# Performance work log

Measured on AMD Instinct MI355X. Metric: run time of the kernel, lower is better.

## Reference

```python
import jax, jax.numpy as jnp
import numpy as np

B, D, K = 32768, 256, 1024


def setup_inputs() -> dict:
    key = jax.random.key(0)
    k1, k2 = jax.random.split(key)
    embedding = jax.random.normal(k1, (B, D), dtype=jnp.float32)
    codebook = jax.random.normal(k2, (K, D), dtype=jnp.float32)
    return {"embedding": embedding, "codebook": codebook}


def reference(embedding, codebook):
    # code_norms: (K,) squared L2 norm of each code
    code_norms = jnp.sum(codebook ** 2, axis=1)            # (K,)
    dots = embedding @ codebook.T                           # (B, K)
    alpha = dots / code_norms[None, :]                      # (B, K)
    # error for projecting e onto line of code c:
    #   ||e - alpha c||^2 = ||e||^2 - dots^2 / ||c||^2
    # (identical math to materializing (B,K,D) diff, without the blowup)
    e_norms = jnp.sum(embedding ** 2, axis=1, keepdims=True)  # (B, 1)
    errors = e_norms - dots ** 2 / code_norms[None, :]        # (B, K)
    indices = jnp.argmin(errors, axis=1)                      # (B,)
    # gather chosen projection: alpha[b, idx[b]] * codebook[idx[b]]
    alpha_sel = jnp.take_along_axis(alpha, indices[:, None], axis=1)  # (B, 1)
    z_out = alpha_sel * codebook[indices]                     # (B, D)
    return (z_out, indices)
```

## Files before the change

kernel.cpp:

```cpp
#include <hip/hip_runtime.h>
#include <cstdint>

#define B_ROWS 32768
#define DIM    256
#define KCODES 1024
#define NSPLIT 2

typedef _Float16 f16x8 __attribute__((ext_vector_type(8)));
typedef float    f32x4 __attribute__((ext_vector_type(4)));


__global__ __launch_bounds__(64) void vq_prep(const float* __restrict__ cb,
                                              _Float16* __restrict__ hi,
                                              _Float16* __restrict__ lo,
                                              float* __restrict__ inv_norm) {
  const int k = blockIdx.x;
  const int lane = threadIdx.x;
  float4 c = reinterpret_cast<const float4*>(cb)[k * 64 + lane];
  float nrm = c.x * c.x + c.y * c.y + c.z * c.z + c.w * c.w;
#pragma unroll
  for (int off = 32; off; off >>= 1) nrm += __shfl_xor(nrm, off);
  if (lane == 0) inv_norm[k] = 1.0f / nrm;

  float f[4] = {c.x, c.y, c.z, c.w};
  _Float16 h[4], l[4];
#pragma unroll
  for (int i = 0; i < 4; ++i) {
    h[i] = (_Float16)f[i];
    l[i] = (_Float16)((f[i] - (float)h[i]) * 2048.0f);
  }
  const int phys = (lane >> 1) ^ (k & 15);
  const int byteoff = k * 512 + phys * 16 + (lane & 1) * 8;
  *reinterpret_cast<uint2*>((char*)hi + byteoff) = *reinterpret_cast<uint2*>(h);
  *reinterpret_cast<uint2*>((char*)lo + byteoff) = *reinterpret_cast<uint2*>(l);
}

__device__ __forceinline__ void gld16(const void* g, void* l) {
  __builtin_amdgcn_global_load_lds(
      (const __attribute__((address_space(1))) uint32_t*)g,
      (__attribute__((address_space(3))) uint32_t*)l, 16, 0, 0);
}

__global__ __launch_bounds__(256, 1) void vq_main(const float* __restrict__ emb,
                                                  const _Float16* __restrict__ cbh,
                                                  const _Float16* __restrict__ cbl,
                                                  const float* __restrict__ inv_g,
                                                  float2* __restrict__ cand) {
  __shared__ uint4 Btile[2][1024];
  __shared__ float inv_s[KCODES];

  const int flat = threadIdx.x;
  const int wave = flat >> 6;
  const int lane = flat & 63;
  const int quad = lane >> 4;
  const int lr   = lane & 15;

  const int split  = blockIdx.x & (NSPLIT - 1);
  const int rowblk = blockIdx.x >> 1;
  const int t0 = split * 32;

  reinterpret_cast<float4*>(inv_s)[flat] = reinterpret_cast<const float4*>(inv_g)[flat];

  f16x8 Ah[4][8], Al[4][8];
  const int row0 = rowblk * 256 + wave * 64;
#pragma unroll
  for (int s = 0; s < 4; ++s) {
    const float* rp = emb + (size_t)(row0 + s * 16 + lr) * DIM;
#pragma unroll
    for (int c = 0; c < 8; ++c) {
      const float* p = rp + c * 32 + quad * 8;
      float4 f0 = *reinterpret_cast<const float4*>(p);
      float4 f1 = *reinterpret_cast<const float4*>(p + 4);
      float f[8] = {f0.x, f0.y, f0.z, f0.w, f1.x, f1.y, f1.z, f1.w};
      f16x8 h, l;
#pragma unroll
      for (int j = 0; j < 8; ++j) {
        _Float16 hv = (_Float16)f[j];
        h[j] = hv;
        l[j] = (_Float16)((f[j] - (float)hv) * 2048.0f);
      }
      Ah[s][c] = h;
      Al[s][c] = l;
    }
  }

  auto stage = [&](int buf, int t) {
    const char* srcH = (const char*)cbh + t * 8192;
    const char* srcL = (const char*)cbl + t * 8192;
    char* dst = (char*)&Btile[buf][0];
    const int off = flat * 16;
    gld16(srcH + off,        dst + off);
    gld16(srcH + 4096 + off, dst + 4096 + off);
    gld16(srcL + off,        dst + 8192 + off);
    gld16(srcL + 4096 + off, dst + 12288 + off);
  };
  stage(0, t0);

  float bg[16], bd[16];
  int   bk[16];
#pragma unroll
  for (int i = 0; i < 16; ++i) { bg[i] = -1.0f; bd[i] = 0.0f; bk[i] = t0 * 16; }

  auto comp = [&](const char* buf, f32x4* aA, f32x4* aB) {
#pragma unroll
    for (int s = 0; s < 4; ++s) {
      aA[s] = (f32x4){0, 0, 0, 0};
      aB[s] = (f32x4){0, 0, 0, 0};
    }
#pragma unroll
    for (int c = 0; c < 8; ++c) {
      const int g = (((c * 4 + quad) ^ lr) * 16) + lr * 512;
      f16x8 bh = *reinterpret_cast<const f16x8*>(buf + g);
      f16x8 bl = *reinterpret_cast<const f16x8*>(buf + 8192 + g);
#pragma unroll
      for (int s = 0; s < 4; ++s) {
        aA[s] = __builtin_amdgcn_mfma_f32_16x16x32_f16(Ah[s][c], bh, aA[s], 0, 0, 0);
        aB[s] = __builtin_amdgcn_mfma_f32_16x16x32_f16(Al[s][c], bh, aB[s], 0, 0, 0);
        aB[s] = __builtin_amdgcn_mfma_f32_16x16x32_f16(Ah[s][c], bl, aB[s], 0, 0, 0);
      }
    }
  };

  auto epi = [&](const f32x4* aA, const f32x4* aB, int t) {
    const int n = t * 16 + lr;
    const float inl = inv_s[n];
#pragma unroll
    for (int s = 0; s < 4; ++s)
#pragma unroll
      for (int r = 0; r < 4; ++r) {
        float d = fmaf(aB[s][r], 4.8828125e-4f, aA[s][r]);
        float g = d * d * inl;
        const int i = (s << 2) | r;
        if (g > bg[i]) { bg[i] = g; bd[i] = d; bk[i] = n; }
      }
  };

  f32x4 aA0[4], aB0[4], aA1[4], aB1[4];
  for (int tt = 0; tt < 32; tt += 2) {
    __syncthreads();
    stage(1, t0 + tt + 1);
    comp((const char*)&Btile[0][0], aA0, aB0);
    if (tt) epi(aA1, aB1, t0 + tt - 1);
    __syncthreads();
    if (tt + 2 < 32) stage(0, t0 + tt + 2);
    comp((const char*)&Btile[1][0], aA1, aB1);
    epi(aA0, aB0, t0 + tt);
  }
  epi(aA1, aB1, t0 + 31);

#pragma unroll
  for (int s = 0; s < 4; ++s) {
#pragma unroll
    for (int r = 0; r < 4; ++r) {
      const int i = (s << 2) | r;
      float g = bg[i]; int k = bk[i]; float d = bd[i];
#pragma unroll
      for (int m = 1; m < 16; m <<= 1) {
        float g2 = __shfl_xor(g, m);
        int   k2 = __shfl_xor(k, m);
        float d2 = __shfl_xor(d, m);
        if (g2 > g || (g2 == g && k2 < k)) { g = g2; k = k2; d = d2; }
      }
      if (lr == 0) {
        const int row = row0 + s * 16 + quad * 4 + r;
        cand[(size_t)split * B_ROWS + row] = make_float2(d, __int_as_float(k));
      }
    }
  }
}

__global__ __launch_bounds__(256) void vq_reduce(const float2* __restrict__ cand,
                                                 const float* __restrict__ inv_g,
                                                 const float* __restrict__ cb,
                                                 float* __restrict__ out) {
  const int wave = threadIdx.x >> 6;
  const int lane = threadIdx.x & 63;
  const int row = blockIdx.x * 4 + wave;

  float best_g = -1.0f, best_d = 0.0f;
  int best_k = 0;
#pragma unroll
  for (int s = 0; s < NSPLIT; ++s) {
    float2 c = cand[(size_t)s * B_ROWS + row];
    int k = __float_as_int(c.y);
    float g = c.x * c.x * inv_g[k];
    if (g > best_g || (g == best_g && k < best_k)) {
      best_g = g; best_d = c.x; best_k = k;
    }
  }
  const float alpha = best_d * inv_g[best_k];
  float4 c4 = reinterpret_cast<const float4*>(cb)[best_k * 64 + lane];
  float4 z = {alpha * c4.x, alpha * c4.y, alpha * c4.z, alpha * c4.w};
  reinterpret_cast<float4*>(out)[(size_t)row * 64 + lane] = z;
  if (lane == 0) out[(size_t)B_ROWS * DIM + row] = (float)best_k;
}

extern "C" void kernel_launch(void* const* d_in, const int* in_sizes, int n_in,
                              void* d_out, int out_size, void* d_ws, size_t ws_size,
                              hipStream_t stream) {
  const float* emb = (const float*)d_in[0];
  const float* cb  = (const float*)d_in[1];
  _Float16* cbh = (_Float16*)d_ws;
  _Float16* cbl = (_Float16*)((char*)d_ws + (512 << 10));
  float*    inv = (float*)((char*)d_ws + (1 << 20));
  float2*   cand = (float2*)((char*)d_ws + (1 << 20) + 4096);

  vq_prep<<<KCODES, 64, 0, stream>>>(cb, cbh, cbl, inv);
  vq_main<<<(B_ROWS / 256) * NSPLIT, 256, 0, stream>>>(emb, cbh, cbl, inv, cand);
  vq_reduce<<<B_ROWS / 4, 256, 0, stream>>>(cand, inv, cb, (float*)d_out);
}
```

Before: 158.3 us.

## Pre-normalize codebook, drop per-code scaling, double tile size and split accumulators

The codebook is pre-scaled by 1/||c|| in the prep kernel, so the main kernel compares squared dots directly. This removes the inverse-norm shared table and its per-tile multiply, and the reduce kernel rescales alpha using the stored inverse sqrt norm. The main loop now stages 32 codes per barrier instead of 16, halving the number of syncs. It also uses three independent accumulator chains instead of two to shorten MFMA dependency chains. The trade-offs are a larger LDS footprint, extra accumulator registers, and slightly different rounding from normalizing before the fp16 hi/lo split.

```diff
diff --git a/kernel.cpp b/kernel.cpp
--- a/kernel.cpp
+++ b/kernel.cpp
@@ -13,16 +13,17 @@
 __global__ __launch_bounds__(64) void vq_prep(const float* __restrict__ cb,
                                               _Float16* __restrict__ hi,
                                               _Float16* __restrict__ lo,
-                                              float* __restrict__ inv_norm) {
+                                              float* __restrict__ ivs) {
   const int k = blockIdx.x;
   const int lane = threadIdx.x;
   float4 c = reinterpret_cast<const float4*>(cb)[k * 64 + lane];
   float nrm = c.x * c.x + c.y * c.y + c.z * c.z + c.w * c.w;
 #pragma unroll
   for (int off = 32; off; off >>= 1) nrm += __shfl_xor(nrm, off);
-  if (lane == 0) inv_norm[k] = 1.0f / nrm;
-
-  float f[4] = {c.x, c.y, c.z, c.w};
+  const float invn = 1.0f / sqrtf(nrm);
+  if (lane == 0) ivs[k] = invn;
+
+  float f[4] = {c.x * invn, c.y * invn, c.z * invn, c.w * invn};
   _Float16 h[4], l[4];
 #pragma unroll
   for (int i = 0; i < 4; ++i) {
@@ -44,10 +45,8 @@
 __global__ __launch_bounds__(256, 1) void vq_main(const float* __restrict__ emb,
                                                   const _Float16* __restrict__ cbh,
                                                   const _Float16* __restrict__ cbl,
-                                                  const float* __restrict__ inv_g,
                                                   float2* __restrict__ cand) {
-  __shared__ uint4 Btile[2][1024];
-  __shared__ float inv_s[KCODES];
+  __shared__ uint4 Btile[2][2048];
 
   const int flat = threadIdx.x;
   const int wave = flat >> 6;
@@ -57,9 +56,7 @@
 
   const int split  = blockIdx.x & (NSPLIT - 1);
   const int rowblk = blockIdx.x >> 1;
-  const int t0 = split * 32;
-
-  reinterpret_cast<float4*>(inv_s)[flat] = reinterpret_cast<const float4*>(inv_g)[flat];
+  const int code0  = split * 512;
 
   f16x8 Ah[4][8], Al[4][8];
   const int row0 = rowblk * 256 + wave * 64;
@@ -84,69 +81,68 @@
     }
   }
 
-  auto stage = [&](int buf, int t) {
-    const char* srcH = (const char*)cbh + t * 8192;
-    const char* srcL = (const char*)cbl + t * 8192;
+  auto stage = [&](int buf, int ch) {
+    const int cbase = code0 + ch * 32;
     char* dst = (char*)&Btile[buf][0];
-    const int off = flat * 16;
-    gld16(srcH + off,        dst + off);
-    gld16(srcH + 4096 + off, dst + 4096 + off);
-    gld16(srcL + off,        dst + 8192 + off);
-    gld16(srcL + 4096 + off, dst + 12288 + off);
+    const int off = wave * 2048 + lane * 16;
+#pragma unroll
+    for (int r = 0; r < 4; ++r) {
+      const char* src = (const char*)((r & 1) ? cbl : cbh) + (cbase + (r >> 1) * 16) * 512;
+      gld16(src + off,        dst + r * 8192 + off);
+      gld16(src + off + 1024, dst + r * 8192 + off + 1024);
+    }
   };
-  stage(0, t0);
+  stage(0, 0);
 
   float bg[16], bd[16];
   int   bk[16];
 #pragma unroll
-  for (int i = 0; i < 16; ++i) { bg[i] = -1.0f; bd[i] = 0.0f; bk[i] = t0 * 16; }
-
-  auto comp = [&](const char* buf, f32x4* aA, f32x4* aB) {
-#pragma unroll
-    for (int s = 0; s < 4; ++s) {
-      aA[s] = (f32x4){0, 0, 0, 0};
-      aB[s] = (f32x4){0, 0, 0, 0};
-    }
-#pragma unroll
-    for (int c = 0; c < 8; ++c) {
-      const int g = (((c * 4 + quad) ^ lr) * 16) + lr * 512;
-      f16x8 bh = *reinterpret_cast<const f16x8*>(buf + g);
-      f16x8 bl = *reinterpret_cast<const f16x8*>(buf + 8192 + g);
+  for (int i = 0; i < 16; ++i) { bg[i] = -1.0f; bd[i] = 0.0f; bk[i] = code0; }
+
+  __syncthreads();
+  for (int ch = 0; ch < 16; ++ch) {
+    const char* base = (const char*)&Btile[ch & 1][0];
+    if (ch + 1 < 16) stage((ch + 1) & 1, ch + 1);
+
+#pragma unroll
+    for (int tt = 0; tt < 2; ++tt) {
+      f32x4 aA[4], aB[4], aC[4];
 #pragma unroll
       for (int s = 0; s < 4; ++s) {
-        aA[s] = __builtin_amdgcn_mfma_f32_16x16x32_f16(Ah[s][c], bh, aA[s], 0, 0, 0);
-        aB[s] = __builtin_amdgcn_mfma_f32_16x16x32_f16(Al[s][c], bh, aB[s], 0, 0, 0);
-        aB[s] = __builtin_amdgcn_mfma_f32_16x16x32_f16(Ah[s][c], bl, aB[s], 0, 0, 0);
-      }
-    }
-  };
-
-  auto epi = [&](const f32x4* aA, const f32x4* aB, int t) {
-    const int n = t * 16 + lr;
-    const float inl = inv_s[n];
-#pragma unroll
-    for (int s = 0; s < 4; ++s)
-#pragma unroll
-      for (int r = 0; r < 4; ++r) {
-        float d = fmaf(aB[s][r], 4.8828125e-4f, aA[s][r]);
-        float g = d * d * inl;
-        const int i = (s << 2) | r;
-        if (g > bg[i]) { bg[i] = g; bd[i] = d; bk[i] = n; }
-      }
-  };
-
-  f32x4 aA0[4], aB0[4], aA1[4], aB1[4];
-  for (int tt = 0; tt < 32; tt += 2) {
-    __syncthreads();
-    stage(1, t0 + tt + 1);
-    comp((const char*)&Btile[0][0], aA0, aB0);
-    if (tt) epi(aA1, aB1, t0 + tt - 1);
-    __syncthreads();
-    if (tt + 2 < 32) stage(0, t0 + tt + 2);
-    comp((const char*)&Btile[1][0], aA1, aB1);
-    epi(aA0, aB0, t0 + tt);
-  }
-  epi(aA1, aB1, t0 + 31);
+        aA[s] = (f32x4){0, 0, 0, 0};
+        aB[s] = (f32x4){0, 0, 0, 0};
+        aC[s] = (f32x4){0, 0, 0, 0};
+      }
+#pragma unroll
+      for (int c = 0; c < 8; ++c) {
+        const int g = (((c * 4 + quad) ^ lr) * 16) + lr * 512;
+        f16x8 bh = *reinterpret_cast<const f16x8*>(base + tt * 16384 + g);
+        f16x8 bl = *reinterpret_cast<const f16x8*>(base + tt * 16384 + 8192 + g);
+#pragma unroll
+        for (int s = 0; s < 4; ++s)
+          aA[s] = __builtin_amdgcn_mfma_f32_16x16x32_f16(Ah[s][c], bh, aA[s], 0, 0, 0);
+#pragma unroll
+        for (int s = 0; s < 4; ++s)
+          aB[s] = __builtin_amdgcn_mfma_f32_16x16x32_f16(Al[s][c], bh, aB[s], 0, 0, 0);
+#pragma unroll
+        for (int s = 0; s < 4; ++s)
+          aC[s] = __builtin_amdgcn_mfma_f32_16x16x32_f16(Ah[s][c], bl, aC[s], 0, 0, 0);
+      }
+
+      const int n = code0 + ch * 32 + tt * 16 + lr;
+#pragma unroll
+      for (int s = 0; s < 4; ++s)
+#pragma unroll
+        for (int r = 0; r < 4; ++r) {
+          float x = aB[s][r] + aC[s][r];
+          float d = fmaf(x, 4.8828125e-4f, aA[s][r]);
+          float g = d * d;
+          const int i = (s << 2) | r;
+          if (g > bg[i]) { bg[i] = g; bd[i] = d; bk[i] = n; }
+        }
+    }
+    if (ch + 1 < 16) __syncthreads();
+  }
 
 #pragma unroll
   for (int s = 0; s < 4; ++s) {
@@ -170,7 +166,7 @@
 }
 
 __global__ __launch_bounds__(256) void vq_reduce(const float2* __restrict__ cand,
-                                                 const float* __restrict__ inv_g,
+                                                 const float* __restrict__ ivs,
                                                  const float* __restrict__ cb,
                                                  float* __restrict__ out) {
   const int wave = threadIdx.x >> 6;
@@ -183,12 +179,12 @@
   for (int s = 0; s < NSPLIT; ++s) {
     float2 c = cand[(size_t)s * B_ROWS + row];
     int k = __float_as_int(c.y);
-    float g = c.x * c.x * inv_g[k];
+    float g = c.x * c.x;
     if (g > best_g || (g == best_g && k < best_k)) {
       best_g = g; best_d = c.x; best_k = k;
     }
   }
-  const float alpha = best_d * inv_g[best_k];
+  const float alpha = best_d * ivs[best_k];
   float4 c4 = reinterpret_cast<const float4*>(cb)[best_k * 64 + lane];
   float4 z = {alpha * c4.x, alpha * c4.y, alpha * c4.z, alpha * c4.w};
   reinterpret_cast<float4*>(out)[(size_t)row * 64 + lane] = z;
@@ -202,10 +198,10 @@
   const float* cb  = (const float*)d_in[1];
   _Float16* cbh = (_Float16*)d_ws;
   _Float16* cbl = (_Float16*)((char*)d_ws + (512 << 10));
-  float*    inv = (float*)((char*)d_ws + (1 << 20));
+  float*    ivs = (float*)((char*)d_ws + (1 << 20));
   float2*   cand = (float2*)((char*)d_ws + (1 << 20) + 4096);
 
-  vq_prep<<<KCODES, 64, 0, stream>>>(cb, cbh, cbl, inv);
-  vq_main<<<(B_ROWS / 256) * NSPLIT, 256, 0, stream>>>(emb, cbh, cbl, inv, cand);
-  vq_reduce<<<B_ROWS / 4, 256, 0, stream>>>(cand, inv, cb, (float*)d_out);
-}
+  vq_prep<<<KCODES, 64, 0, stream>>>(cb, cbh, cbl, ivs);
+  vq_main<<<(B_ROWS / 256) * NSPLIT, 256, 0, stream>>>(emb, cbh, cbl, cand);
+  vq_reduce<<<B_ROWS / 4, 256, 0, stream>>>(cand, ivs, cb, (float*)d_out);
+}
```

Result: no change. 157.9 us (-0.3%).
